# Kernel optimization log

Hardware: AMD Instinct MI355X
Metric: run time of the kernel (lower is better)

The kernel has to match this reference:

```python
import jax, jax.numpy as jnp
import numpy as np

INPUT_SIZE = 2048
HIDDEN_SIZE = 2048
BATCH = 4096


def setup_inputs() -> dict:
    key = jax.random.key(0)
    ks = jax.random.split(key, 12)
    std = 1.0 / HIDDEN_SIZE ** 0.5
    def u(k, shape):
        return jax.random.uniform(k, shape, jnp.float32, -std, std)
    inp = {
        "x": jax.random.normal(ks[0], (BATCH, INPUT_SIZE), jnp.float32),
        "h": jax.random.normal(ks[1], (BATCH, HIDDEN_SIZE), jnp.float32),
        "c": jax.random.normal(ks[2], (BATCH, HIDDEN_SIZE), jnp.float32),
        "weight_ii": u(ks[3], (HIDDEN_SIZE, INPUT_SIZE)),
        "weight_if": u(ks[4], (HIDDEN_SIZE, INPUT_SIZE)),
        "weight_ig": u(ks[5], (HIDDEN_SIZE, INPUT_SIZE)),
        "weight_io": u(ks[6], (HIDDEN_SIZE, INPUT_SIZE)),
        "weight_hi": u(ks[7], (HIDDEN_SIZE, HIDDEN_SIZE)),
        "weight_hf": u(ks[8], (HIDDEN_SIZE, HIDDEN_SIZE)),
        "weight_hg": u(ks[9], (HIDDEN_SIZE, HIDDEN_SIZE)),
        "weight_ho": u(ks[10], (HIDDEN_SIZE, HIDDEN_SIZE)),
        "bias_i": u(ks[11], (HIDDEN_SIZE,)),
        "bias_f": u(jax.random.fold_in(key, 100), (HIDDEN_SIZE,)),
        "bias_g": u(jax.random.fold_in(key, 101), (HIDDEN_SIZE,)),
        "bias_o": u(jax.random.fold_in(key, 102), (HIDDEN_SIZE,)),
    }
    return inp


def reference(x, h, c, weight_ii, weight_if, weight_ig, weight_io,
              weight_hi, weight_hf, weight_hg, weight_ho,
              bias_i, bias_f, bias_g, bias_o):
    # Fuse the 4 input projections and 4 hidden projections into 2 GEMMs
    # (same math as 8 separate matmuls in the original module).
    W_x = jnp.concatenate([weight_ii, weight_if, weight_ig, weight_io], axis=0)  # [4H, I]
    W_h = jnp.concatenate([weight_hi, weight_hf, weight_hg, weight_ho], axis=0)  # [4H, H]
    b = jnp.concatenate([bias_i, bias_f, bias_g, bias_o], axis=0)                # [4H]
    gates = x @ W_x.T + h @ W_h.T + b                                            # [B, 4H]
    gi, gf, gg, go = jnp.split(gates, 4, axis=1)
    i = jax.nn.sigmoid(gi)
    f = jax.nn.sigmoid(gf)
    g = jnp.tanh(gg)
    o = jax.nn.sigmoid(go)
    c_new = f * c + i * g
    h_new = o * jnp.tanh(c_new)
    return (h_new, c_new)
```

## Files before the change

kernel.cpp:

```cpp
#include <hip/hip_runtime.h>
#include <cstdint>
#include <cstddef>

#define BATCH 4096
#define HID   2048

typedef __attribute__((ext_vector_type(8))) short bf16x8;
typedef __attribute__((ext_vector_type(4))) float f32x4;

__device__ __forceinline__ unsigned short f2bf(float f) {
  union { float f; unsigned u; } a; a.f = f;
  unsigned u = a.u;
  return (unsigned short)((u + 0x7FFFu + ((u >> 16) & 1u)) >> 16);
}

__device__ __forceinline__ void gload_lds16(const void* g, void* l) {
  __builtin_amdgcn_global_load_lds((const __attribute__((address_space(1))) void*)g,
                                   (__attribute__((address_space(3))) void*)l, 16, 0, 0);
}

#define SCHED0() __builtin_amdgcn_sched_barrier(0)
#define SBAR()  do { SCHED0(); __builtin_amdgcn_s_barrier(); SCHED0(); } while (0)
#define WAITV(N) do { SCHED0(); asm volatile("s_waitcnt vmcnt(" #N ")" ::: "memory"); SCHED0(); } while (0)
#define WAITL(N) do { SCHED0(); asm volatile("s_waitcnt lgkmcnt(" #N ")" ::: "memory"); SCHED0(); } while (0)
#define DSR(dst, adr, IMM) asm volatile("ds_read_b128 %0, %1 offset:" #IMM : "=v"(dst) : "v"(adr))

#define RD_A2(ADR) do { DSR(a2[0],ADR,4096); DSR(a2[1],ADR,5120); DSR(a2[2],ADR,6144); DSR(a2[3],ADR,7168); } while (0)
#define RD_N(AADR,BADR,A1,BF) do { \
  DSR(A1[0],AADR,0); DSR(A1[1],AADR,1024); DSR(A1[2],AADR,2048); DSR(A1[3],AADR,3072); \
  DSR(BF[0],BADR,0); DSR(BF[1],BADR,1024); DSR(BF[2],BADR,2048); DSR(BF[3],BADR,3072); } while (0)

#define MFMA_LO(A1, BF) do { _Pragma("unroll") \
  for (int m_ = 0; m_ < 4; m_++) { _Pragma("unroll") \
    for (int n_ = 0; n_ < 4; n_++) \
      acc[m_][n_] = __builtin_amdgcn_mfma_f32_16x16x32_bf16(A1[m_], BF[n_], acc[m_][n_], 0, 0, 0); } } while (0)
#define MFMA_HI(BF) do { _Pragma("unroll") \
  for (int m_ = 0; m_ < 4; m_++) { _Pragma("unroll") \
    for (int n_ = 0; n_ < 4; n_++) \
      acc[4+m_][n_] = __builtin_amdgcn_mfma_f32_16x16x32_bf16(a2[m_], BF[n_], acc[4+m_][n_], 0, 0, 0); } } while (0)

#define STAGE_G(KOFF, DOF) do { \
  gload_lds16(pA + (KOFF), dA + (DOF)); \
  gload_lds16(pA + 128*4096 + (KOFF), dA + (DOF) + 8192); \
  gload_lds16(pB + (KOFF), dA + (DOF) + 16384); \
  gload_lds16(pB + 32*4096 + (KOFF), dA + (DOF) + 24576); } while (0)

#define ADVR(o) do { (o) += 32768; if ((o) == 163840) (o) = 0; } while (0)

#define SLOT(VN, SA, SB, STG, MA1, MBF) do { \
  WAITV(VN); \
  SBAR(); \
  { unsigned aC_ = aBase + (unsigned)o_c; RD_A2(aC_); } \
  { unsigned aN_ = aBase + (unsigned)o_n, bN_ = bBase + (unsigned)o_n; RD_N(aN_, bN_, SA, SB); } \
  STG; \
  WAITL(12); \
  __builtin_amdgcn_s_setprio(1); MFMA_LO(MA1, MBF); __builtin_amdgcn_s_setprio(0); \
  WAITL(8); \
  __builtin_amdgcn_s_setprio(1); MFMA_HI(MBF); __builtin_amdgcn_s_setprio(0); \
  ADVR(o_c); ADVR(o_n); ADVR(o_s); koff += 32; \
} while (0)

__global__ __launch_bounds__(256) void convert_kernel(
    const float* __restrict__ x, const float* __restrict__ h,
    const float* __restrict__ wii, const float* __restrict__ wif,
    const float* __restrict__ wig, const float* __restrict__ wio,
    const float* __restrict__ whi, const float* __restrict__ whf,
    const float* __restrict__ whg, const float* __restrict__ who,
    unsigned short* __restrict__ Abf, unsigned short* __restrict__ Wbf) {
  int seg = blockIdx.y;
  const float* src;
  unsigned short* dst;
  int ofs;
  size_t rofs;
  if (seg < 4) {
    src = (seg < 2) ? x : h;
    dst = Abf;
    ofs = (seg < 2) ? 0 : 2048;
    rofs = (seg & 1) ? 2048 : 0;
    src += rofs * 2048;
  } else {
    int g = (seg - 4) & 3;
    dst = Wbf + (size_t)g * 2048 * 4096;
    ofs = (seg >= 8) ? 2048 : 0;
    rofs = 0;
    switch (seg) {
      case 4: src = wii; break; case 5: src = wif; break;
      case 6: src = wig; break; case 7: src = wio; break;
      case 8: src = whi; break; case 9: src = whf; break;
      case 10: src = whg; break; default: src = who; break;
    }
  }
  size_t idx = (size_t)blockIdx.x * 256 + threadIdx.x;
  size_t e = idx * 4;
  int n = (int)(e >> 11);
  int k = (int)(e & 2047);
  float4 v = *(const float4*)(src + e);
  ushort4 o;
  o.x = f2bf(v.x); o.y = f2bf(v.y); o.z = f2bf(v.z); o.w = f2bf(v.w);
  *(ushort4*)(dst + (rofs + (size_t)n) * 4096 + ofs + k) = o;
}

__global__ __launch_bounds__(512, 2) void lstm_gemm8(
    const unsigned short* __restrict__ Abf, const unsigned short* __restrict__ Wbf,
    const float* __restrict__ c_in,
    const float* __restrict__ bias_i, const float* __restrict__ bias_f,
    const float* __restrict__ bias_g, const float* __restrict__ bias_o,
    float* __restrict__ out) {
  __shared__ unsigned short lds[5 * 16384];

  int tid = threadIdx.x;
  int lane = tid & 63;
  int wid = tid >> 6;
  int wr = wid >> 2;
  int wc = wid & 3;
  int lrow = lane & 15;
  int qh = lane >> 4;

  int bid = blockIdx.x;
  int xcd = bid & 7;
  int t7 = bid >> 3;
  int mt = t7 & 15;
  int bn = xcd * 4 + (t7 >> 4);
  int m0 = mt * 256;

  int r0 = tid >> 2, cc0 = tid & 3;
  int ccs0 = cc0 ^ ((r0 >> 1) & 3);
  const unsigned short* pA = Abf + (size_t)(m0 + r0) * 4096 + ccs0 * 8;
  int g0 = (r0 >> 4) & 3;
  int jw = bn * 64 + ((r0 >> 6) & 3) * 16 + (r0 & 15);
  const unsigned short* pB = Wbf + ((size_t)g0 * 2048 + jw) * 4096 + ccs0 * 8;

  char* L0 = (char*)&lds[0];
  char* dA = L0 + tid * 16;
  unsigned ldsOff = (unsigned)(size_t)(__attribute__((address_space(3))) char*)L0;

  int arow0 = wr * 128 + lrow;
  int brow0 = wc * 64 + lrow;
  unsigned qsA = ((unsigned)(qh ^ ((arow0 >> 1) & 3))) << 4;
  unsigned qsB = ((unsigned)(qh ^ ((brow0 >> 1) & 3))) << 4;
  unsigned aBase = ldsOff + (unsigned)arow0 * 64 + qsA;
  unsigned bBase = ldsOff + 16384u + (unsigned)brow0 * 64 + qsB;

  f32x4 acc[8][4];
  #pragma unroll
  for (int a = 0; a < 8; a++)
    #pragma unroll
    for (int b = 0; b < 4; b++) acc[a][b] = (f32x4){0.f, 0.f, 0.f, 0.f};

  bf16x8 a1A[4], bfA[4], a1B[4], bfB[4], a2[4];

  int o_c = 0, o_n = 32768, o_s = 131072;
  int koff = 128;

  STAGE_G(0, 0);
  STAGE_G(32, 32768);
  STAGE_G(64, 65536);
  STAGE_G(96, 98304);
  WAITV(12);
  SBAR();
  { unsigned aN_ = aBase, bN_ = bBase; RD_N(aN_, bN_, a1A, bfA); }

  for (int i = 0; i < 62; ++i) {
    SLOT(8, a1B, bfB, STAGE_G(koff, o_s), a1A, bfA);
    SLOT(8, a1A, bfA, STAGE_G(koff, o_s), a1B, bfB);
  }

  SLOT(8, a1B, bfB, (void)0, a1A, bfA);
  SLOT(4, a1A, bfA, (void)0, a1B, bfB);
  SLOT(0, a1B, bfB, (void)0, a1A, bfA);
  {
    unsigned aC_ = aBase + (unsigned)o_c;
    RD_A2(aC_);
    WAITL(4);
    __builtin_amdgcn_s_setprio(1); MFMA_LO(a1B, bfB); __builtin_amdgcn_s_setprio(0);
    WAITL(0);
    __builtin_amdgcn_s_setprio(1); MFMA_HI(bfB); __builtin_amdgcn_s_setprio(0);
  }

  int j = bn * 64 + wc * 16 + lrow;
  float bi = bias_i[j], bff = bias_f[j], bgg = bias_g[j], bo = bias_o[j];
  int rbase = m0 + wr * 128 + qh * 4;
  #pragma unroll
  for (int mf = 0; mf < 8; mf++) {
    #pragma unroll
    for (int qq = 0; qq < 4; qq++) {
      int m = rbase + mf * 16 + qq;
      size_t off = (size_t)m * HID + j;
      float gi = acc[mf][0][qq] + bi;
      float gf = acc[mf][1][qq] + bff;
      float gg = acc[mf][2][qq] + bgg;
      float go = acc[mf][3][qq] + bo;
      float iv = 1.f / (1.f + __expf(-gi));
      float fv = 1.f / (1.f + __expf(-gf));
      float gv = tanhf(gg);
      float ov = 1.f / (1.f + __expf(-go));
      float cn = fv * c_in[off] + iv * gv;
      float hn = ov * tanhf(cn);
      out[off] = hn;
      out[(size_t)BATCH * HID + off] = cn;
    }
  }
}

__global__ __launch_bounds__(256) void lstm_gemm_fb(
    const float* __restrict__ x, const float* __restrict__ h,
    const float* __restrict__ wii, const float* __restrict__ wif,
    const float* __restrict__ wig, const float* __restrict__ wio,
    const float* __restrict__ whi, const float* __restrict__ whf,
    const float* __restrict__ whg, const float* __restrict__ who,
    const float* __restrict__ c_in,
    const float* __restrict__ bias_i, const float* __restrict__ bias_f,
    const float* __restrict__ bias_g, const float* __restrict__ bias_o,
    float* __restrict__ out) {
  __shared__ unsigned short Ald[128 * 64];
  __shared__ unsigned short Bld[128 * 64];
  int tid = threadIdx.x;
  int lane = tid & 63;
  int wid = tid >> 6;
  int wr = wid >> 1, wc = wid & 1;
  int bid = blockIdx.x;
  int swz = (bid & 7) * 256 + (bid >> 3);
  int mt = swz & 31;
  int ht = swz >> 5;
  int m0 = mt * 128;
  int j0 = ht * 32;
  f32x4 acc[4][4];
  #pragma unroll
  for (int a = 0; a < 4; a++)
    #pragma unroll
    for (int b = 0; b < 4; b++) acc[a][b] = (f32x4){0.f, 0.f, 0.f, 0.f};
  int lrow = lane & 15;
  int lsw = lrow & 7;
  int qbase = lane >> 4;
  for (int kt = 0; kt < 64; kt++) {
    int k0 = kt * 64;
    const float* Asrc = (k0 < 2048) ? x : h;
    int ka = k0 & 2047;
    #pragma unroll
    for (int i = 0; i < 4; i++) {
      int c = i * 256 + tid;
      int r = c >> 3, cc = c & 7;
      int ccs = cc ^ (r & 7);
      const float* s = Asrc + (size_t)(m0 + r) * 2048 + ka + ccs * 8;
      float4 v0 = *(const float4*)s;
      float4 v1 = *(const float4*)(s + 4);
      bf16x8 pk;
      pk[0] = (short)f2bf(v0.x); pk[1] = (short)f2bf(v0.y);
      pk[2] = (short)f2bf(v0.z); pk[3] = (short)f2bf(v0.w);
      pk[4] = (short)f2bf(v1.x); pk[5] = (short)f2bf(v1.y);
      pk[6] = (short)f2bf(v1.z); pk[7] = (short)f2bf(v1.w);
      *(bf16x8*)((char*)Ald + (size_t)c * 16) = pk;
    }
    #pragma unroll
    for (int i = 0; i < 4; i++) {
      int c = i * 256 + tid;
      int rb = c >> 3, cc = c & 7;
      int ccs = cc ^ (rb & 7);
      int g = rb >> 5, jj = rb & 31;
      const float* Bsrc;
      if (k0 < 2048) Bsrc = (g == 0) ? wii : (g == 1) ? wif : (g == 2) ? wig : wio;
      else           Bsrc = (g == 0) ? whi : (g == 1) ? whf : (g == 2) ? whg : who;
      const float* s = Bsrc + (size_t)(j0 + jj) * 2048 + ka + ccs * 8;
      float4 v0 = *(const float4*)s;
      float4 v1 = *(const float4*)(s + 4);
      bf16x8 pk;
      pk[0] = (short)f2bf(v0.x); pk[1] = (short)f2bf(v0.y);
      pk[2] = (short)f2bf(v0.z); pk[3] = (short)f2bf(v0.w);
      pk[4] = (short)f2bf(v1.x); pk[5] = (short)f2bf(v1.y);
      pk[6] = (short)f2bf(v1.z); pk[7] = (short)f2bf(v1.w);
      *(bf16x8*)((char*)Bld + (size_t)c * 16) = pk;
    }
    __syncthreads();
    #pragma unroll
    for (int ks = 0; ks < 2; ks++) {
      int q = ks * 4 + qbase;
      int qs8 = (q ^ lsw) * 8;
      bf16x8 af[4], bg[4];
      #pragma unroll
      for (int mf = 0; mf < 4; mf++)
        af[mf] = *(const bf16x8*)&Ald[(wr * 64 + mf * 16 + lrow) * 64 + qs8];
      #pragma unroll
      for (int g = 0; g < 4; g++)
        bg[g] = *(const bf16x8*)&Bld[(g * 32 + wc * 16 + lrow) * 64 + qs8];
      #pragma unroll
      for (int mf = 0; mf < 4; mf++)
        #pragma unroll
        for (int g = 0; g < 4; g++)
          acc[mf][g] = __builtin_amdgcn_mfma_f32_16x16x32_bf16(af[mf], bg[g], acc[mf][g], 0, 0, 0);
    }
    __syncthreads();
  }
  int j = j0 + wc * 16 + lrow;
  float bi = bias_i[j], bff = bias_f[j], bgg = bias_g[j], bo = bias_o[j];
  int rbase = m0 + wr * 64 + (lane >> 4) * 4;
  #pragma unroll
  for (int mf = 0; mf < 4; mf++) {
    #pragma unroll
    for (int q = 0; q < 4; q++) {
      int m = rbase + mf * 16 + q;
      size_t off = (size_t)m * HID + j;
      float gi = acc[mf][0][q] + bi;
      float gf = acc[mf][1][q] + bff;
      float gg = acc[mf][2][q] + bgg;
      float go = acc[mf][3][q] + bo;
      float iv = 1.f / (1.f + __expf(-gi));
      float fv = 1.f / (1.f + __expf(-gf));
      float gv = tanhf(gg);
      float ov = 1.f / (1.f + __expf(-go));
      float cn = fv * c_in[off] + iv * gv;
      float hn = ov * tanhf(cn);
      out[off] = hn;
      out[(size_t)BATCH * HID + off] = cn;
    }
  }
}

extern "C" void kernel_launch(void* const* d_in, const int* in_sizes, int n_in,
                              void* d_out, int out_size, void* d_ws, size_t ws_size,
                              hipStream_t stream) {
  const float* x   = (const float*)d_in[0];
  const float* h   = (const float*)d_in[1];
  const float* c   = (const float*)d_in[2];
  const float* wii = (const float*)d_in[3];
  const float* wif = (const float*)d_in[4];
  const float* wig = (const float*)d_in[5];
  const float* wio = (const float*)d_in[6];
  const float* whi = (const float*)d_in[7];
  const float* whf = (const float*)d_in[8];
  const float* whg = (const float*)d_in[9];
  const float* who = (const float*)d_in[10];
  const float* bi  = (const float*)d_in[11];
  const float* bf  = (const float*)d_in[12];
  const float* bg  = (const float*)d_in[13];
  const float* bo  = (const float*)d_in[14];
  float* out = (float*)d_out;

  size_t needA = (size_t)4096 * 4096 * 2;
  size_t needW = (size_t)8192 * 4096 * 2;

  if (ws_size >= needA + needW) {
    unsigned short* Abf = (unsigned short*)d_ws;
    unsigned short* Wbf = (unsigned short*)((char*)d_ws + needA);
    convert_kernel<<<dim3(4096, 12), 256, 0, stream>>>(
        x, h, wii, wif, wig, wio, whi, whf, whg, who, Abf, Wbf);
    lstm_gemm8<<<512, 512, 0, stream>>>(Abf, Wbf, c, bi, bf, bg, bo, out);
  } else {
    lstm_gemm_fb<<<2048, 256, 0, stream>>>(
        x, h, wii, wif, wig, wio, whi, whf, whg, who,
        c, bi, bf, bg, bo, out);
  }
}
```

Measured before the change: 321.2 us.

## Switch LSTM GEMM to 4 waves with 128x128 per-wave tiles

Rewrites the main bf16 GEMM kernel to use 256 threads (4 waves, 2x2) with each wave computing a 128x128 output tile (8x8 MFMA fragments), instead of 8 waves each doing 128x64. The LDS ring drops from 5 to 4 stages and the pipeline is simplified to a full-register double buffer of 16 ds_reads per k-step, with a full lgkmcnt wait before each read batch. The aim is more MFMA work per LDS read and fewer waves contending, at the cost of higher register pressure (256 accumulator floats per lane), one block per CU, and less latency hiding from wave-level parallelism.

New measurement: 354.7 us. 10.5% more time.

```diff
diff --git a/kernel.cpp b/kernel.cpp
--- a/kernel.cpp
+++ b/kernel.cpp
@@ -25,38 +25,41 @@
 #define WAITL(N) do { SCHED0(); asm volatile("s_waitcnt lgkmcnt(" #N ")" ::: "memory"); SCHED0(); } while (0)
 #define DSR(dst, adr, IMM) asm volatile("ds_read_b128 %0, %1 offset:" #IMM : "=v"(dst) : "v"(adr))
 
-#define RD_A2(ADR) do { DSR(a2[0],ADR,4096); DSR(a2[1],ADR,5120); DSR(a2[2],ADR,6144); DSR(a2[3],ADR,7168); } while (0)
-#define RD_N(AADR,BADR,A1,BF) do { \
-  DSR(A1[0],AADR,0); DSR(A1[1],AADR,1024); DSR(A1[2],AADR,2048); DSR(A1[3],AADR,3072); \
-  DSR(BF[0],BADR,0); DSR(BF[1],BADR,1024); DSR(BF[2],BADR,2048); DSR(BF[3],BADR,3072); } while (0)
-
-#define MFMA_LO(A1, BF) do { _Pragma("unroll") \
-  for (int m_ = 0; m_ < 4; m_++) { _Pragma("unroll") \
-    for (int n_ = 0; n_ < 4; n_++) \
-      acc[m_][n_] = __builtin_amdgcn_mfma_f32_16x16x32_bf16(A1[m_], BF[n_], acc[m_][n_], 0, 0, 0); } } while (0)
-#define MFMA_HI(BF) do { _Pragma("unroll") \
-  for (int m_ = 0; m_ < 4; m_++) { _Pragma("unroll") \
-    for (int n_ = 0; n_ < 4; n_++) \
-      acc[4+m_][n_] = __builtin_amdgcn_mfma_f32_16x16x32_bf16(a2[m_], BF[n_], acc[4+m_][n_], 0, 0, 0); } } while (0)
+#define RD16(AS, BS) do { \
+  unsigned aA_ = aBase + (unsigned)o_n, bB_ = bBase + (unsigned)o_n; \
+  DSR(AS[0],aA_,0);    DSR(AS[1],aA_,1024); DSR(AS[2],aA_,2048); DSR(AS[3],aA_,3072); \
+  DSR(AS[4],aA_,4096); DSR(AS[5],aA_,5120); DSR(AS[6],aA_,6144); DSR(AS[7],aA_,7168); \
+  DSR(BS[0],bB_,0);    DSR(BS[1],bB_,1024); DSR(BS[2],bB_,2048); DSR(BS[3],bB_,3072); \
+  DSR(BS[4],bB_,4096); DSR(BS[5],bB_,5120); DSR(BS[6],bB_,6144); DSR(BS[7],bB_,7168); \
+} while (0)
+
+#define MFMA64(AS, BS) do { _Pragma("unroll") \
+  for (int m_ = 0; m_ < 8; m_++) { _Pragma("unroll") \
+    for (int n_ = 0; n_ < 8; n_++) \
+      acc[m_][n_] = __builtin_amdgcn_mfma_f32_16x16x32_bf16(AS[m_], BS[n_], acc[m_][n_], 0, 0, 0); } \
+} while (0)
 
 #define STAGE_G(KOFF, DOF) do { \
-  gload_lds16(pA + (KOFF), dA + (DOF)); \
-  gload_lds16(pA + 128*4096 + (KOFF), dA + (DOF) + 8192); \
-  gload_lds16(pB + (KOFF), dA + (DOF) + 16384); \
-  gload_lds16(pB + 32*4096 + (KOFF), dA + (DOF) + 24576); } while (0)
-
-#define ADVR(o) do { (o) += 32768; if ((o) == 163840) (o) = 0; } while (0)
-
-#define SLOT(VN, SA, SB, STG, MA1, MBF) do { \
-  WAITV(VN); \
+  gload_lds16(pA + (KOFF),          dA + (DOF)); \
+  gload_lds16(pA + 262144 + (KOFF), dA + (DOF) + 4096); \
+  gload_lds16(pA + 524288 + (KOFF), dA + (DOF) + 8192); \
+  gload_lds16(pA + 786432 + (KOFF), dA + (DOF) + 12288); \
+  gload_lds16(pB + (KOFF),          dA + (DOF) + 16384); \
+  gload_lds16(pB + 65536 + (KOFF),  dA + (DOF) + 20480); \
+  gload_lds16(pB + 131072 + (KOFF), dA + (DOF) + 24576); \
+  gload_lds16(pB + 196608 + (KOFF), dA + (DOF) + 28672); \
+} while (0)
+
+#define ADVR(o) do { (o) = ((o) + 32768) & 131071; } while (0)
+
+#define SLOT(VW, STG, ACUR, BCUR, ANXT, BNXT) do { \
+  VW; \
   SBAR(); \
-  { unsigned aC_ = aBase + (unsigned)o_c; RD_A2(aC_); } \
-  { unsigned aN_ = aBase + (unsigned)o_n, bN_ = bBase + (unsigned)o_n; RD_N(aN_, bN_, SA, SB); } \
+  WAITL(0); \
+  RD16(ANXT, BNXT); \
   STG; \
-  WAITL(12); \
-  __builtin_amdgcn_s_setprio(1); MFMA_LO(MA1, MBF); __builtin_amdgcn_s_setprio(0); \
-  WAITL(8); \
-  __builtin_amdgcn_s_setprio(1); MFMA_HI(MBF); __builtin_amdgcn_s_setprio(0); \
+  SCHED0(); \
+  __builtin_amdgcn_s_setprio(1); MFMA64(ACUR, BCUR); __builtin_amdgcn_s_setprio(0); \
   ADVR(o_c); ADVR(o_n); ADVR(o_s); koff += 32; \
 } while (0)
 
@@ -100,19 +103,19 @@
   *(ushort4*)(dst + (rofs + (size_t)n) * 4096 + ofs + k) = o;
 }
 
-__global__ __launch_bounds__(512, 2) void lstm_gemm8(
+__global__ __launch_bounds__(256, 1) void lstm_gemm4(
     const unsigned short* __restrict__ Abf, const unsigned short* __restrict__ Wbf,
     const float* __restrict__ c_in,
     const float* __restrict__ bias_i, const float* __restrict__ bias_f,
     const float* __restrict__ bias_g, const float* __restrict__ bias_o,
     float* __restrict__ out) {
-  __shared__ unsigned short lds[5 * 16384];
+  __shared__ unsigned short lds[4 * 16384];
 
   int tid = threadIdx.x;
   int lane = tid & 63;
   int wid = tid >> 6;
-  int wr = wid >> 2;
-  int wc = wid & 3;
+  int wr = wid >> 1;
+  int wc = wid & 1;
   int lrow = lane & 15;
   int qh = lane >> 4;
 
@@ -127,77 +130,69 @@
   int ccs0 = cc0 ^ ((r0 >> 1) & 3);
   const unsigned short* pA = Abf + (size_t)(m0 + r0) * 4096 + ccs0 * 8;
   int g0 = (r0 >> 4) & 3;
-  int jw = bn * 64 + ((r0 >> 6) & 3) * 16 + (r0 & 15);
-  const unsigned short* pB = Wbf + ((size_t)g0 * 2048 + jw) * 4096 + ccs0 * 8;
+  const unsigned short* pB = Wbf + ((size_t)g0 * 2048 + bn * 64 + (r0 & 15)) * 4096 + ccs0 * 8;
 
   char* L0 = (char*)&lds[0];
   char* dA = L0 + tid * 16;
   unsigned ldsOff = (unsigned)(size_t)(__attribute__((address_space(3))) char*)L0;
 
-  int arow0 = wr * 128 + lrow;
-  int brow0 = wc * 64 + lrow;
-  unsigned qsA = ((unsigned)(qh ^ ((arow0 >> 1) & 3))) << 4;
-  unsigned qsB = ((unsigned)(qh ^ ((brow0 >> 1) & 3))) << 4;
-  unsigned aBase = ldsOff + (unsigned)arow0 * 64 + qsA;
-  unsigned bBase = ldsOff + 16384u + (unsigned)brow0 * 64 + qsB;
-
-  f32x4 acc[8][4];
+  unsigned qs = ((unsigned)(qh ^ ((lrow >> 1) & 3))) << 4;
+  unsigned aBase = ldsOff + (unsigned)(wr * 128 + lrow) * 64 + qs;
+  unsigned bBase = ldsOff + 16384u + (unsigned)(wc * 128 + lrow) * 64 + qs;
+
+  f32x4 acc[8][8];
   #pragma unroll
   for (int a = 0; a < 8; a++)
     #pragma unroll
-    for (int b = 0; b < 4; b++) acc[a][b] = (f32x4){0.f, 0.f, 0.f, 0.f};
-
-  bf16x8 a1A[4], bfA[4], a1B[4], bfB[4], a2[4];
-
-  int o_c = 0, o_n = 32768, o_s = 131072;
-  int koff = 128;
+    for (int b = 0; b < 8; b++) acc[a][b] = (f32x4){0.f, 0.f, 0.f, 0.f};
+
+  bf16x8 aA[8], bA[8], aB[8], bB[8];
+
+  int o_c = 0, o_n = 32768, o_s = 98304;
+  int koff = 96;
 
   STAGE_G(0, 0);
   STAGE_G(32, 32768);
   STAGE_G(64, 65536);
-  STAGE_G(96, 98304);
-  WAITV(12);
+  WAITV(16);
   SBAR();
-  { unsigned aN_ = aBase, bN_ = bBase; RD_N(aN_, bN_, a1A, bfA); }
+  { int sv = o_n; o_n = 0; RD16(aA, bA); o_n = sv; }
 
   for (int i = 0; i < 62; ++i) {
-    SLOT(8, a1B, bfB, STAGE_G(koff, o_s), a1A, bfA);
-    SLOT(8, a1A, bfA, STAGE_G(koff, o_s), a1B, bfB);
-  }
-
-  SLOT(8, a1B, bfB, (void)0, a1A, bfA);
-  SLOT(4, a1A, bfA, (void)0, a1B, bfB);
-  SLOT(0, a1B, bfB, (void)0, a1A, bfA);
-  {
-    unsigned aC_ = aBase + (unsigned)o_c;
-    RD_A2(aC_);
-    WAITL(4);
-    __builtin_amdgcn_s_setprio(1); MFMA_LO(a1B, bfB); __builtin_amdgcn_s_setprio(0);
-    WAITL(0);
-    __builtin_amdgcn_s_setprio(1); MFMA_HI(bfB); __builtin_amdgcn_s_setprio(0);
-  }
-
-  int j = bn * 64 + wc * 16 + lrow;
-  float bi = bias_i[j], bff = bias_f[j], bgg = bias_g[j], bo = bias_o[j];
+    SLOT(WAITV(8), STAGE_G(koff, o_s), aA, bA, aB, bB);
+    SLOT(WAITV(8), STAGE_G(koff, o_s), aB, bB, aA, bA);
+  }
+  SLOT(WAITV(8), STAGE_G(koff, o_s), aA, bA, aB, bB);
+  SLOT(WAITV(8), (void)0, aB, bB, aA, bA);
+  SLOT(WAITV(0), (void)0, aA, bA, aB, bB);
+  WAITL(0);
+  __builtin_amdgcn_s_setprio(1); MFMA64(aB, bB); __builtin_amdgcn_s_setprio(0);
+
+  int jb = bn * 64 + wc * 32 + lrow;
   int rbase = m0 + wr * 128 + qh * 4;
   #pragma unroll
-  for (int mf = 0; mf < 8; mf++) {
-    #pragma unroll
-    for (int qq = 0; qq < 4; qq++) {
-      int m = rbase + mf * 16 + qq;
-      size_t off = (size_t)m * HID + j;
-      float gi = acc[mf][0][qq] + bi;
-      float gf = acc[mf][1][qq] + bff;
-      float gg = acc[mf][2][qq] + bgg;
-      float go = acc[mf][3][qq] + bo;
-      float iv = 1.f / (1.f + __expf(-gi));
-      float fv = 1.f / (1.f + __expf(-gf));
-      float gv = tanhf(gg);
-      float ov = 1.f / (1.f + __expf(-go));
-      float cn = fv * c_in[off] + iv * gv;
-      float hn = ov * tanhf(cn);
-      out[off] = hn;
-      out[(size_t)BATCH * HID + off] = cn;
+  for (int jj2 = 0; jj2 < 2; jj2++) {
+    int j = jb + jj2 * 16;
+    float bi = bias_i[j], bff = bias_f[j], bgg = bias_g[j], bo = bias_o[j];
+    #pragma unroll
+    for (int mf = 0; mf < 8; mf++) {
+      #pragma unroll
+      for (int qq = 0; qq < 4; qq++) {
+        int m = rbase + mf * 16 + qq;
+        size_t off = (size_t)m * HID + j;
+        float gi = acc[mf][jj2 * 4 + 0][qq] + bi;
+        float gf = acc[mf][jj2 * 4 + 1][qq] + bff;
+        float gg = acc[mf][jj2 * 4 + 2][qq] + bgg;
+        float go = acc[mf][jj2 * 4 + 3][qq] + bo;
+        float iv = 1.f / (1.f + __expf(-gi));
+        float fv = 1.f / (1.f + __expf(-gf));
+        float gv = tanhf(gg);
+        float ov = 1.f / (1.f + __expf(-go));
+        float cn = fv * c_in[off] + iv * gv;
+        float hn = ov * tanhf(cn);
+        out[off] = hn;
+        out[(size_t)BATCH * HID + off] = cn;
+      }
     }
   }
 }
@@ -343,7 +338,7 @@
     unsigned short* Wbf = (unsigned short*)((char*)d_ws + needA);
     convert_kernel<<<dim3(4096, 12), 256, 0, stream>>>(
         x, h, wii, wif, wig, wio, whi, whf, whg, who, Abf, Wbf);
-    lstm_gemm8<<<512, 512, 0, stream>>>(Abf, Wbf, c, bi, bf, bg, bo, out);
+    lstm_gemm4<<<512, 256, 0, stream>>>(Abf, Wbf, c, bi, bf, bg, bo, out);
   } else {
     lstm_gemm_fb<<<2048, 256, 0, stream>>>(
         x, h, wii, wif, wig, wio, whi, whf, whg, who,
```

## Restructure GEMM mainloop to double-buffered BK=64 with quarter-step MFMA interleaving

Applied to the files above, without the earlier changes.

Replaces the 5-stage ring of BK=32 LDS buffers with two 64-wide K buffers, using an 8-chunk XOR swizzle. The main loop is split into quarter-steps that each issue a partial set of LDS reads, stage half of the next tile's A or B loads, and run an MFMA block. The aim is fewer barriers per K and better overlap of global loads with MFMA work. In exchange it adds many more s_barrier and lgkmcnt(0) waits per iteration and gives shallower prefetch depth, which could expose load latency.

Measured after the change: 308.5 us. 3.9% less time.

```diff
diff --git a/kernel.cpp b/kernel.cpp
--- a/kernel.cpp
+++ b/kernel.cpp
@@ -25,40 +25,35 @@
 #define WAITL(N) do { SCHED0(); asm volatile("s_waitcnt lgkmcnt(" #N ")" ::: "memory"); SCHED0(); } while (0)
 #define DSR(dst, adr, IMM) asm volatile("ds_read_b128 %0, %1 offset:" #IMM : "=v"(dst) : "v"(adr))
 
-#define RD_A2(ADR) do { DSR(a2[0],ADR,4096); DSR(a2[1],ADR,5120); DSR(a2[2],ADR,6144); DSR(a2[3],ADR,7168); } while (0)
-#define RD_N(AADR,BADR,A1,BF) do { \
-  DSR(A1[0],AADR,0); DSR(A1[1],AADR,1024); DSR(A1[2],AADR,2048); DSR(A1[3],AADR,3072); \
-  DSR(BF[0],BADR,0); DSR(BF[1],BADR,1024); DSR(BF[2],BADR,2048); DSR(BF[3],BADR,3072); } while (0)
-
-#define MFMA_LO(A1, BF) do { _Pragma("unroll") \
-  for (int m_ = 0; m_ < 4; m_++) { _Pragma("unroll") \
-    for (int n_ = 0; n_ < 4; n_++) \
-      acc[m_][n_] = __builtin_amdgcn_mfma_f32_16x16x32_bf16(A1[m_], BF[n_], acc[m_][n_], 0, 0, 0); } } while (0)
-#define MFMA_HI(BF) do { _Pragma("unroll") \
-  for (int m_ = 0; m_ < 4; m_++) { _Pragma("unroll") \
-    for (int n_ = 0; n_ < 4; n_++) \
-      acc[4+m_][n_] = __builtin_amdgcn_mfma_f32_16x16x32_bf16(a2[m_], BF[n_], acc[4+m_][n_], 0, 0, 0); } } while (0)
-
-#define STAGE_G(KOFF, DOF) do { \
-  gload_lds16(pA + (KOFF), dA + (DOF)); \
-  gload_lds16(pA + 128*4096 + (KOFF), dA + (DOF) + 8192); \
-  gload_lds16(pB + (KOFF), dA + (DOF) + 16384); \
-  gload_lds16(pB + 32*4096 + (KOFF), dA + (DOF) + 24576); } while (0)
-
-#define ADVR(o) do { (o) += 32768; if ((o) == 163840) (o) = 0; } while (0)
-
-#define SLOT(VN, SA, SB, STG, MA1, MBF) do { \
-  WAITV(VN); \
-  SBAR(); \
-  { unsigned aC_ = aBase + (unsigned)o_c; RD_A2(aC_); } \
-  { unsigned aN_ = aBase + (unsigned)o_n, bN_ = bBase + (unsigned)o_n; RD_N(aN_, bN_, SA, SB); } \
-  STG; \
-  WAITL(12); \
-  __builtin_amdgcn_s_setprio(1); MFMA_LO(MA1, MBF); __builtin_amdgcn_s_setprio(0); \
-  WAITL(8); \
-  __builtin_amdgcn_s_setprio(1); MFMA_HI(MBF); __builtin_amdgcn_s_setprio(0); \
-  ADVR(o_c); ADVR(o_n); ADVR(o_s); koff += 32; \
-} while (0)
+#define RD_A_MH0(A0, A1) do { \
+  DSR(aS[0],A0,0);    DSR(aS[1],A1,0);    DSR(aS[2],A0,2048);  DSR(aS[3],A1,2048); \
+  DSR(aS[4],A0,4096); DSR(aS[5],A1,4096); DSR(aS[6],A0,6144);  DSR(aS[7],A1,6144); } while (0)
+#define RD_A_MH1(A0, A1) do { \
+  DSR(aS[0],A0,8192);  DSR(aS[1],A1,8192);  DSR(aS[2],A0,10240); DSR(aS[3],A1,10240); \
+  DSR(aS[4],A0,12288); DSR(aS[5],A1,12288); DSR(aS[6],A0,14336); DSR(aS[7],A1,14336); } while (0)
+#define RD_B0(B0, B1) do { \
+  DSR(bS0[0],B0,0); DSR(bS0[1],B1,0); DSR(bS0[2],B0,2048); DSR(bS0[3],B1,2048); } while (0)
+#define RD_B1(B0, B1) do { \
+  DSR(bS1[0],B0,4096); DSR(bS1[1],B1,4096); DSR(bS1[2],B0,6144); DSR(bS1[3],B1,6144); } while (0)
+
+#define MFMAQ(AS, BS, MO, NO) do { \
+  _Pragma("unroll") \
+  for (int mf_ = 0; mf_ < 4; mf_++) { \
+    _Pragma("unroll") \
+    for (int nf_ = 0; nf_ < 2; nf_++) { \
+      acc[(MO)+mf_][(NO)+nf_] = __builtin_amdgcn_mfma_f32_16x16x32_bf16(AS[2*mf_],   BS[2*nf_],   acc[(MO)+mf_][(NO)+nf_], 0, 0, 0); \
+      acc[(MO)+mf_][(NO)+nf_] = __builtin_amdgcn_mfma_f32_16x16x32_bf16(AS[2*mf_+1], BS[2*nf_+1], acc[(MO)+mf_][(NO)+nf_], 0, 0, 0); \
+    } } } while (0)
+
+#define PRIO1() __builtin_amdgcn_s_setprio(1)
+#define PRIO0() __builtin_amdgcn_s_setprio(0)
+
+#define ST_AH(BUF, H, KO) do { \
+  gload_lds16(pA0 + (size_t)(H) * 524288 + (KO),          dD + (BUF) * 65536 + (H) * 16384); \
+  gload_lds16(pA0 + (size_t)(H) * 524288 + 262144 + (KO), dD + (BUF) * 65536 + (H) * 16384 + 8192); } while (0)
+#define ST_BH(BUF, H, KO) do { \
+  gload_lds16(pB0 + (size_t)(H) * 131072 + (KO),         dD + (BUF) * 65536 + 32768 + (H) * 16384); \
+  gload_lds16(pB0 + (size_t)(H) * 131072 + 65536 + (KO), dD + (BUF) * 65536 + 32768 + (H) * 16384 + 8192); } while (0)
 
 __global__ __launch_bounds__(256) void convert_kernel(
     const float* __restrict__ x, const float* __restrict__ h,
@@ -106,7 +101,7 @@
     const float* __restrict__ bias_i, const float* __restrict__ bias_f,
     const float* __restrict__ bias_g, const float* __restrict__ bias_o,
     float* __restrict__ out) {
-  __shared__ unsigned short lds[5 * 16384];
+  __shared__ unsigned short lds[2 * 32768];
 
   int tid = threadIdx.x;
   int lane = tid & 63;
@@ -123,23 +118,25 @@
   int bn = xcd * 4 + (t7 >> 4);
   int m0 = mt * 256;
 
-  int r0 = tid >> 2, cc0 = tid & 3;
-  int ccs0 = cc0 ^ ((r0 >> 1) & 3);
-  const unsigned short* pA = Abf + (size_t)(m0 + r0) * 4096 + ccs0 * 8;
+  int r0 = tid >> 3, cc0 = tid & 7;
+  int ccs0 = cc0 ^ (r0 & 7);
+  const unsigned short* pA0 = Abf + (size_t)(m0 + r0) * 4096 + ccs0 * 8;
   int g0 = (r0 >> 4) & 3;
-  int jw = bn * 64 + ((r0 >> 6) & 3) * 16 + (r0 & 15);
-  const unsigned short* pB = Wbf + ((size_t)g0 * 2048 + jw) * 4096 + ccs0 * 8;
+  const unsigned short* pB0 = Wbf + ((size_t)g0 * 2048 + bn * 64 + (r0 & 15)) * 4096 + ccs0 * 8;
 
   char* L0 = (char*)&lds[0];
-  char* dA = L0 + tid * 16;
+  char* dD = L0 + tid * 16;
   unsigned ldsOff = (unsigned)(size_t)(__attribute__((address_space(3))) char*)L0;
 
-  int arow0 = wr * 128 + lrow;
-  int brow0 = wc * 64 + lrow;
-  unsigned qsA = ((unsigned)(qh ^ ((arow0 >> 1) & 3))) << 4;
-  unsigned qsB = ((unsigned)(qh ^ ((brow0 >> 1) & 3))) << 4;
-  unsigned aBase = ldsOff + (unsigned)arow0 * 64 + qsA;
-  unsigned bBase = ldsOff + 16384u + (unsigned)brow0 * 64 + qsB;
+  int key = lrow & 7;
+  unsigned c0 = (unsigned)(qh ^ key) * 16u;
+  unsigned c1 = c0 ^ 64u;
+  unsigned aRow = (unsigned)(wr * 128 + lrow) * 128u;
+  unsigned bRow = 32768u + (unsigned)(wc * 64 + lrow) * 128u;
+  unsigned aAd00 = ldsOff + aRow + c0, aAd01 = ldsOff + aRow + c1;
+  unsigned aAd10 = aAd00 + 65536u,     aAd11 = aAd01 + 65536u;
+  unsigned bAd00 = ldsOff + bRow + c0, bAd01 = ldsOff + bRow + c1;
+  unsigned bAd10 = bAd00 + 65536u,     bAd11 = bAd01 + 65536u;
 
   f32x4 acc[8][4];
   #pragma unroll
@@ -147,34 +144,92 @@
     #pragma unroll
     for (int b = 0; b < 4; b++) acc[a][b] = (f32x4){0.f, 0.f, 0.f, 0.f};
 
-  bf16x8 a1A[4], bfA[4], a1B[4], bfB[4], a2[4];
-
-  int o_c = 0, o_n = 32768, o_s = 131072;
-  int koff = 128;
-
-  STAGE_G(0, 0);
-  STAGE_G(32, 32768);
-  STAGE_G(64, 65536);
-  STAGE_G(96, 98304);
-  WAITV(12);
+  bf16x8 aS[8], bS0[4], bS1[4];
+
+  ST_AH(0, 0, 0); ST_AH(0, 1, 0);
+  ST_BH(0, 0, 0); ST_BH(0, 1, 0);
+  ST_BH(1, 0, 64); ST_BH(1, 1, 64);
+  WAITV(4);
   SBAR();
-  { unsigned aN_ = aBase, bN_ = bBase; RD_N(aN_, bN_, a1A, bfA); }
-
-  for (int i = 0; i < 62; ++i) {
-    SLOT(8, a1B, bfB, STAGE_G(koff, o_s), a1A, bfA);
-    SLOT(8, a1A, bfA, STAGE_G(koff, o_s), a1B, bfB);
-  }
-
-  SLOT(8, a1B, bfB, (void)0, a1A, bfA);
-  SLOT(4, a1A, bfA, (void)0, a1B, bfB);
-  SLOT(0, a1B, bfB, (void)0, a1A, bfA);
+
+  for (int i = 0; i < 31; ++i) {
+    int koO = i * 128 + 64;
+    int koN = i * 128 + 128;
+    int koN2 = i * 128 + 192;
+    RD_A_MH0(aAd00, aAd01); RD_B0(bAd00, bAd01);
+    ST_AH(1, 0, koO);
+    SBAR(); WAITL(0);
+    PRIO1(); MFMAQ(aS, bS0, 0, 0); PRIO0();
+    SBAR();
+    RD_B1(bAd00, bAd01);
+    ST_AH(1, 1, koO);
+    SBAR(); WAITL(0);
+    PRIO1(); MFMAQ(aS, bS1, 0, 2); PRIO0();
+    SBAR();
+    RD_A_MH1(aAd00, aAd01);
+    ST_BH(0, 0, koN);
+    SBAR(); WAITL(0);
+    PRIO1(); MFMAQ(aS, bS0, 4, 0); PRIO0();
+    SBAR();
+    ST_BH(0, 1, koN);
+    SBAR();
+    PRIO1(); MFMAQ(aS, bS1, 4, 2); PRIO0();
+    WAITV(4);
+    SBAR();
+    RD_A_MH0(aAd10, aAd11); RD_B0(bAd10, bAd11);
+    ST_AH(0, 0, koN);
+    SBAR(); WAITL(0);
+    PRIO1(); MFMAQ(aS, bS0, 0, 0); PRIO0();
+    SBAR();
+    RD_B1(bAd10, bAd11);
+    ST_AH(0, 1, koN);
+    SBAR(); WAITL(0);
+    PRIO1(); MFMAQ(aS, bS1, 0, 2); PRIO0();
+    SBAR();
+    RD_A_MH1(aAd10, aAd11);
+    ST_BH(1, 0, koN2);
+    SBAR(); WAITL(0);
+    PRIO1(); MFMAQ(aS, bS0, 4, 0); PRIO0();
+    SBAR();
+    ST_BH(1, 1, koN2);
+    SBAR();
+    PRIO1(); MFMAQ(aS, bS1, 4, 2); PRIO0();
+    WAITV(4);
+    SBAR();
+  }
+
   {
-    unsigned aC_ = aBase + (unsigned)o_c;
-    RD_A2(aC_);
-    WAITL(4);
-    __builtin_amdgcn_s_setprio(1); MFMA_LO(a1B, bfB); __builtin_amdgcn_s_setprio(0);
-    WAITL(0);
-    __builtin_amdgcn_s_setprio(1); MFMA_HI(bfB); __builtin_amdgcn_s_setprio(0);
+    RD_A_MH0(aAd00, aAd01); RD_B0(bAd00, bAd01);
+    ST_AH(1, 0, 4032);
+    SBAR(); WAITL(0);
+    PRIO1(); MFMAQ(aS, bS0, 0, 0); PRIO0();
+    SBAR();
+    RD_B1(bAd00, bAd01);
+    ST_AH(1, 1, 4032);
+    SBAR(); WAITL(0);
+    PRIO1(); MFMAQ(aS, bS1, 0, 2); PRIO0();
+    SBAR();
+    RD_A_MH1(aAd00, aAd01);
+    SBAR(); WAITL(0);
+    PRIO1(); MFMAQ(aS, bS0, 4, 0); PRIO0();
+    SBAR();
+    SBAR();
+    PRIO1(); MFMAQ(aS, bS1, 4, 2); PRIO0();
+    WAITV(0);
+    SBAR();
+    RD_A_MH0(aAd10, aAd11); RD_B0(bAd10, bAd11);
+    SBAR(); WAITL(0);
+    PRIO1(); MFMAQ(aS, bS0, 0, 0); PRIO0();
+    SBAR();
+    RD_B1(bAd10, bAd11);
+    SBAR(); WAITL(0);
+    PRIO1(); MFMAQ(aS, bS1, 0, 2); PRIO0();
+    SBAR();
+    RD_A_MH1(aAd10, aAd11);
+    SBAR(); WAITL(0);
+    PRIO1(); MFMAQ(aS, bS0, 4, 0); PRIO0();
+    SBAR();
+    PRIO1(); MFMAQ(aS, bS1, 4, 2); PRIO0();
   }
 
   int j = bn * 64 + wc * 16 + lrow;
```

## Replace deep register/LDS software pipeline with simpler two-stage interval loop

Applied to the files above, without the earlier changes.

Replaces the 5-slot LDS ring with 3-deep prefetch and double-buffered register fragments by a loop that waits for all global loads, barriers once per two k-steps, reads a full fragment cluster and waits on all LDS reads before issuing MFMAs. Prefetch depth drops to two stages ahead, and each k-step now fully serializes its LDS reads ahead of its MFMAs. This cuts register pressure and barrier count, but it gives up the overlap between LDS reads, global loads and matrix math that the old schedule had.

After: 318.7 us. About the same (-0.8%).

```diff
diff --git a/kernel.cpp b/kernel.cpp
--- a/kernel.cpp
+++ b/kernel.cpp
@@ -24,40 +24,44 @@
 #define WAITV(N) do { SCHED0(); asm volatile("s_waitcnt vmcnt(" #N ")" ::: "memory"); SCHED0(); } while (0)
 #define WAITL(N) do { SCHED0(); asm volatile("s_waitcnt lgkmcnt(" #N ")" ::: "memory"); SCHED0(); } while (0)
 #define DSR(dst, adr, IMM) asm volatile("ds_read_b128 %0, %1 offset:" #IMM : "=v"(dst) : "v"(adr))
-
-#define RD_A2(ADR) do { DSR(a2[0],ADR,4096); DSR(a2[1],ADR,5120); DSR(a2[2],ADR,6144); DSR(a2[3],ADR,7168); } while (0)
-#define RD_N(AADR,BADR,A1,BF) do { \
-  DSR(A1[0],AADR,0); DSR(A1[1],AADR,1024); DSR(A1[2],AADR,2048); DSR(A1[3],AADR,3072); \
-  DSR(BF[0],BADR,0); DSR(BF[1],BADR,1024); DSR(BF[2],BADR,2048); DSR(BF[3],BADR,3072); } while (0)
-
-#define MFMA_LO(A1, BF) do { _Pragma("unroll") \
-  for (int m_ = 0; m_ < 4; m_++) { _Pragma("unroll") \
+#define PRIO1() __builtin_amdgcn_s_setprio(1)
+#define PRIO0() __builtin_amdgcn_s_setprio(0)
+
+#define READ_CLUSTER(AADR, BADR) do { \
+  DSR(a1[0], (AADR), 0); DSR(a1[1], (AADR), 1024); DSR(a1[2], (AADR), 2048); DSR(a1[3], (AADR), 3072); \
+  DSR(bf_[0], (BADR), 0); DSR(bf_[1], (BADR), 1024); DSR(bf_[2], (BADR), 2048); DSR(bf_[3], (BADR), 3072); \
+  DSR(a2[0], (AADR), 4096); DSR(a2[1], (AADR), 5120); DSR(a2[2], (AADR), 6144); DSR(a2[3], (AADR), 7168); \
+} while (0)
+
+#define MFMA_HALF(AF, OFS) do { \
+  _Pragma("unroll") \
+  for (int m_ = 0; m_ < 4; m_++) { \
+    _Pragma("unroll") \
     for (int n_ = 0; n_ < 4; n_++) \
-      acc[m_][n_] = __builtin_amdgcn_mfma_f32_16x16x32_bf16(A1[m_], BF[n_], acc[m_][n_], 0, 0, 0); } } while (0)
-#define MFMA_HI(BF) do { _Pragma("unroll") \
-  for (int m_ = 0; m_ < 4; m_++) { _Pragma("unroll") \
-    for (int n_ = 0; n_ < 4; n_++) \
-      acc[4+m_][n_] = __builtin_amdgcn_mfma_f32_16x16x32_bf16(a2[m_], BF[n_], acc[4+m_][n_], 0, 0, 0); } } while (0)
+      acc[(OFS) + m_][n_] = __builtin_amdgcn_mfma_f32_16x16x32_bf16(AF[m_], bf_[n_], acc[(OFS) + m_][n_], 0, 0, 0); \
+  } \
+} while (0)
 
 #define STAGE_G(KOFF, DOF) do { \
   gload_lds16(pA + (KOFF), dA + (DOF)); \
-  gload_lds16(pA + 128*4096 + (KOFF), dA + (DOF) + 8192); \
+  gload_lds16(pA + 128 * 4096 + (KOFF), dA + (DOF) + 8192); \
   gload_lds16(pB + (KOFF), dA + (DOF) + 16384); \
-  gload_lds16(pB + 32*4096 + (KOFF), dA + (DOF) + 24576); } while (0)
-
-#define ADVR(o) do { (o) += 32768; if ((o) == 163840) (o) = 0; } while (0)
-
-#define SLOT(VN, SA, SB, STG, MA1, MBF) do { \
-  WAITV(VN); \
+  gload_lds16(pB + 32 * 4096 + (KOFF), dA + (DOF) + 24576); } while (0)
+
+#define ADV2(o) do { (o) += 65536; if ((o) >= 163840) (o) -= 163840; } while (0)
+
+#define INTERVAL(STG1, STG2) do { \
+  WAITV(0); \
   SBAR(); \
-  { unsigned aC_ = aBase + (unsigned)o_c; RD_A2(aC_); } \
-  { unsigned aN_ = aBase + (unsigned)o_n, bN_ = bBase + (unsigned)o_n; RD_N(aN_, bN_, SA, SB); } \
-  STG; \
-  WAITL(12); \
-  __builtin_amdgcn_s_setprio(1); MFMA_LO(MA1, MBF); __builtin_amdgcn_s_setprio(0); \
-  WAITL(8); \
-  __builtin_amdgcn_s_setprio(1); MFMA_HI(MBF); __builtin_amdgcn_s_setprio(0); \
-  ADVR(o_c); ADVR(o_n); ADVR(o_s); koff += 32; \
+  READ_CLUSTER(aB0 + (unsigned)o_a, bB0 + (unsigned)o_a); \
+  STG1; \
+  WAITL(0); \
+  PRIO1(); MFMA_HALF(a1, 0); MFMA_HALF(a2, 4); PRIO0(); \
+  READ_CLUSTER(aB0 + (unsigned)o_b, bB0 + (unsigned)o_b); \
+  STG2; \
+  WAITL(0); \
+  PRIO1(); MFMA_HALF(a1, 0); MFMA_HALF(a2, 4); PRIO0(); \
+  ADV2(o_a); ADV2(o_b); ADV2(o_s1); ADV2(o_s2); ks += 64; \
 } while (0)
 
 __global__ __launch_bounds__(256) void convert_kernel(
@@ -138,8 +142,8 @@
   int brow0 = wc * 64 + lrow;
   unsigned qsA = ((unsigned)(qh ^ ((arow0 >> 1) & 3))) << 4;
   unsigned qsB = ((unsigned)(qh ^ ((brow0 >> 1) & 3))) << 4;
-  unsigned aBase = ldsOff + (unsigned)arow0 * 64 + qsA;
-  unsigned bBase = ldsOff + 16384u + (unsigned)brow0 * 64 + qsB;
+  unsigned aB0 = ldsOff + (unsigned)arow0 * 64 + qsA;
+  unsigned bB0 = ldsOff + 16384u + (unsigned)brow0 * 64 + qsB;
 
   f32x4 acc[8][4];
   #pragma unroll
@@ -147,35 +151,18 @@
     #pragma unroll
     for (int b = 0; b < 4; b++) acc[a][b] = (f32x4){0.f, 0.f, 0.f, 0.f};
 
-  bf16x8 a1A[4], bfA[4], a1B[4], bfB[4], a2[4];
-
-  int o_c = 0, o_n = 32768, o_s = 131072;
-  int koff = 128;
+  bf16x8 a1[4], a2[4], bf_[4];
+
+  int o_a = 0, o_b = 32768, o_s1 = 65536, o_s2 = 98304;
+  int ks = 64;
 
   STAGE_G(0, 0);
   STAGE_G(32, 32768);
-  STAGE_G(64, 65536);
-  STAGE_G(96, 98304);
-  WAITV(12);
-  SBAR();
-  { unsigned aN_ = aBase, bN_ = bBase; RD_N(aN_, bN_, a1A, bfA); }
-
-  for (int i = 0; i < 62; ++i) {
-    SLOT(8, a1B, bfB, STAGE_G(koff, o_s), a1A, bfA);
-    SLOT(8, a1A, bfA, STAGE_G(koff, o_s), a1B, bfB);
-  }
-
-  SLOT(8, a1B, bfB, (void)0, a1A, bfA);
-  SLOT(4, a1A, bfA, (void)0, a1B, bfB);
-  SLOT(0, a1B, bfB, (void)0, a1A, bfA);
-  {
-    unsigned aC_ = aBase + (unsigned)o_c;
-    RD_A2(aC_);
-    WAITL(4);
-    __builtin_amdgcn_s_setprio(1); MFMA_LO(a1B, bfB); __builtin_amdgcn_s_setprio(0);
-    WAITL(0);
-    __builtin_amdgcn_s_setprio(1); MFMA_HI(bfB); __builtin_amdgcn_s_setprio(0);
-  }
+
+  for (int t = 0; t < 63; ++t) {
+    INTERVAL(STAGE_G(ks, o_s1), STAGE_G(ks + 32, o_s2));
+  }
+  INTERVAL((void)0, (void)0);
 
   int j = bn * 64 + wc * 16 + lrow;
   float bi = bias_i[j], bff = bias_f[j], bgg = bias_g[j], bo = bias_o[j];
```
